# Kernel tuning notes

Measured on AMD Instinct MI355X. Metric: run time of the kernel, lower is better.

The kernel has to match this reference:

```python
import jax, jax.numpy as jnp
import numpy as np

# NF4 codebook (bitsandbytes nf4 data type, 16 levels)
NF4_TABLE = np.array([
    -1.0, -0.6961928009986877, -0.5250730514526367, -0.39491748809814453,
    -0.28444138169288635, -0.18477343022823334, -0.09105003625154495, 0.0,
    0.07958029955625534, 0.16093020141124725, 0.24611230194568634,
    0.33791524171829224, 0.44070982933044434, 0.5626170039176941,
    0.7229568362236023, 1.0], dtype=np.float32)

BLOCKSIZE = 64
SCALING = 32.0 / 16.0  # lora_alpha / r


def setup_inputs() -> dict:
    key = jax.random.key(0)
    k1, k2, k3, k4, k5 = jax.random.split(key, 5)
    tokens, in_f, out_f, r = 256, 4096, 11008, 16
    x = jax.random.normal(k1, (tokens, in_f), dtype=jnp.float32)
    q_codes = jax.random.randint(k2, (out_f, in_f), 0, 16, dtype=jnp.int32)
    absmax = jax.random.uniform(k3, (out_f, in_f // BLOCKSIZE), dtype=jnp.float32)
    lora_A = jax.random.normal(k4, (r, in_f), dtype=jnp.float32) * (1.0 / np.sqrt(in_f))
    lora_B = jax.random.normal(k5, (out_f, r), dtype=jnp.float32) * 0.02
    return {"x": x, "q_codes": q_codes, "absmax": absmax,
            "lora_A": lora_A, "lora_B": lora_B}


def reference(x, q_codes, absmax, lora_A, lora_B):
    out_f, in_f = q_codes.shape
    nf4 = jnp.asarray(NF4_TABLE, dtype=x.dtype)
    # Dequantize: codebook lookup, then per-block absmax scale.
    W = nf4[q_codes].reshape(out_f, in_f // BLOCKSIZE, BLOCKSIZE)
    W = (W * absmax[:, :, None]).reshape(out_f, in_f)  # [out_f, in_f]
    # Base 4-bit linear (no bias in bnb Linear4bit default here).
    base = x @ W.T  # [tokens, out_f]
    # LoRA path: dropout p=0 is identity in eval; scaling = alpha/r.
    lora = (x @ lora_A.T) @ lora_B.T  # [tokens, r] -> [tokens, out_f]
    return base + lora * jnp.asarray(SCALING, dtype=x.dtype)
```

## Files before the change

kernel.cpp:

```cpp
#include <hip/hip_runtime.h>
#include <hip/hip_fp16.h>

typedef unsigned int uint;
typedef unsigned short ushort;

typedef __attribute__((ext_vector_type(8))) _Float16 f16x8;
typedef __attribute__((ext_vector_type(4))) float f32x4;

#define TOK 256
#define OUTF 11008
#define INF 4096
#define BM 256
#define BN 64
#define NT2 172

__device__ __constant__ float NF4_TBL[16] = {
    -1.0f, -0.6961928009986877f, -0.5250730514526367f, -0.39491748809814453f,
    -0.28444138169288635f, -0.18477343022823334f, -0.09105003625154495f, 0.0f,
    0.07958029955625534f, 0.16093020141124725f, 0.24611230194568634f,
    0.33791524171829224f, 0.44070982933044434f, 0.5626170039176941f,
    0.7229568362236023f, 1.0f};

__device__ __forceinline__ ushort f2h(float f) {
  return __half_as_ushort(__float2half(f));
}

__device__ __forceinline__ void async_cp16(const void* g, void* l) {
  __builtin_amdgcn_global_load_lds(
      (const __attribute__((address_space(1))) uint*)g,
      (__attribute__((address_space(3))) uint*)l, 16, 0, 0);
}

__global__ void prep_kernel(const int4* __restrict__ qc4, uint* __restrict__ pk,
                            const float4* __restrict__ x4, ushort4* __restrict__ xh4,
                            const float4* __restrict__ lB4, ushort4* __restrict__ lBh4) {
  const int stride = gridDim.x * blockDim.x;
  const int t0 = blockIdx.x * blockDim.x + threadIdx.x;
  for (int d = t0; d < OUTF * INF / 8; d += stride) {
    int4 a = qc4[2 * d];
    int4 b = qc4[2 * d + 1];
    pk[d] = (uint)(a.x & 15) | ((uint)(a.y & 15) << 4) | ((uint)(a.z & 15) << 8) |
            ((uint)(a.w & 15) << 12) | ((uint)(b.x & 15) << 16) | ((uint)(b.y & 15) << 20) |
            ((uint)(b.z & 15) << 24) | ((uint)(b.w & 15) << 28);
  }
  for (int i = t0; i < TOK * INF / 4; i += stride) {
    float4 v = x4[i];
    ushort4 o;
    o.x = f2h(v.x); o.y = f2h(v.y); o.z = f2h(v.z); o.w = f2h(v.w);
    xh4[i] = o;
  }
  for (int i = t0; i < OUTF * 16; i += stride) {
    int n = i >> 4, jq = i & 15;
    ushort4 o = {0, 0, 0, 0};
    if (jq < 4) {
      float4 v = lB4[n * 4 + jq];
      o.x = f2h(v.x); o.y = f2h(v.y); o.z = f2h(v.z); o.w = f2h(v.w);
    }
    lBh4[i] = o;
  }
}

__global__ __launch_bounds__(1024)
void xa_kernel(const float* __restrict__ x, const float* __restrict__ lA,
               ushort* __restrict__ xa2) {
  const int m = blockIdx.x;
  const int t = threadIdx.x;
  const float4* x4 = (const float4*)(x + (size_t)m * INF);
  const float4* lA4 = (const float4*)lA;
  float4 xv = x4[t];
  float acc[16];
#pragma unroll
  for (int j = 0; j < 16; ++j) {
    float4 a = lA4[j * (INF / 4) + t];
    acc[j] = xv.x * a.x + xv.y * a.y + xv.z * a.z + xv.w * a.w;
  }
#pragma unroll
  for (int j = 0; j < 16; ++j)
#pragma unroll
    for (int s = 32; s > 0; s >>= 1) acc[j] += __shfl_xor(acc[j], s, 64);
  __shared__ float red[16][16];
  const int w = t >> 6, l = t & 63;
  if (l == 0) {
#pragma unroll
    for (int j = 0; j < 16; ++j) red[w][j] = acc[j];
  }
  __syncthreads();
  if (t < 64) {
    ushort v = 0;
    if (t < 16) {
      float s = 0.f;
#pragma unroll
      for (int w2 = 0; w2 < 16; ++w2) s += red[w2][t];
      v = f2h(2.0f * s);
    }
    xa2[m * 64 + t] = v;
  }
}

__global__ __launch_bounds__(256, 3)
void gemm_kernel(const uint* __restrict__ pk, const float* __restrict__ am,
                 const ushort* __restrict__ xh, const ushort* __restrict__ lBh,
                 const ushort* __restrict__ xa2, float* __restrict__ dest, int nst) {
  __shared__ ushort Abuf[BM * 64];
  __shared__ ushort Bbuf[64 * 64];
  __shared__ uint Qbuf[512];
  __shared__ float Qax[1024];
  __shared__ __half2 tbl[256];

  const int tid = threadIdx.x;
  const int w = tid >> 6;
  const int l = tid & 63;
  const int chunk = l >> 4;
  const int rlo = l & 15;
  const int split = blockIdx.x / NT2;
  const int ntile = blockIdx.x - split * NT2;
  const int n0 = ntile * BN;
  const int kb0 = split * nst;

  tbl[tid & 255] = __halves2half2(__float2half(NF4_TBL[tid & 15]),
                                  __float2half(NF4_TBL[(tid >> 4) & 15]));

  const int arow = w * 8 + (l >> 3);
  const int acol = ((l & 7) ^ (l >> 3)) << 3;
  int aoff[2][4];
#pragma unroll
  for (int ks2 = 0; ks2 < 2; ++ks2) {
    const int cc = ks2 * 4 + chunk;
#pragma unroll
    for (int mt = 0; mt < 4; ++mt)
      aoff[ks2][mt] = (w * 64 + mt * 16 + rlo) * 64 + ((cc ^ (l & 7)) << 3);
  }

  const int dr = tid & 63;
  const int p7 = dr & 7;
  const int bw0 = dr * 64 + ((w ^ p7) << 3);
  const int bw1 = dr * 64 + (((w + 4) ^ p7) << 3);

  int boff[2][4];
#pragma unroll
  for (int ks2 = 0; ks2 < 2; ++ks2)
#pragma unroll
    for (int nt = 0; nt < 4; ++nt)
      boff[ks2][nt] = (nt * 16 + rlo) * 64 + (((ks2 * 4 + chunk) ^ (rlo & 7)) << 3);

  f32x4 acc[4][4];
#pragma unroll
  for (int mt = 0; mt < 4; ++mt)
#pragma unroll
    for (int nt = 0; nt < 4; ++nt) acc[mt][nt] = (f32x4){0.f, 0.f, 0.f, 0.f};

  if (w == 0) {
#pragma unroll
    for (int j = 0; j < 4; ++j)
      async_cp16(am + (size_t)(n0 + l) * 64 + kb0 + j * 4, (char*)Qax + j * 1024);
#pragma unroll
    for (int j = 0; j < 2; ++j)
      async_cp16((const char*)pk + (size_t)(n0 + l) * 2048 + kb0 * 32 + j * 16,
                 (char*)Qbuf + j * 1024);
  }
#pragma unroll
  for (int i = 0; i < 8; ++i) {
    const ushort* g = xh + (size_t)(i * 32 + arow) * INF + kb0 * 64 + acol;
    async_cp16(g, &Abuf[(i * 256 + w * 64) * 8]);
  }

  for (int s = 0; s < nst; ++s) {
    __syncthreads();

    uint q0 = Qbuf[dr * 4 + w];
    uint q1 = Qbuf[256 + dr * 4 + w];
    const int sl = s & 15;
    __half2 ax2 = __float2half2_rn(Qax[(sl >> 2) * 256 + dr * 4 + (sl & 3)]);
    {
      union { __half2 h[4]; f16x8 v; } u;
      u.h[0] = __hmul2(tbl[q0 & 255], ax2);
      u.h[1] = __hmul2(tbl[(q0 >> 8) & 255], ax2);
      u.h[2] = __hmul2(tbl[(q0 >> 16) & 255], ax2);
      u.h[3] = __hmul2(tbl[q0 >> 24], ax2);
      *(f16x8*)&Bbuf[bw0] = u.v;
    }
    {
      union { __half2 h[4]; f16x8 v; } u;
      u.h[0] = __hmul2(tbl[q1 & 255], ax2);
      u.h[1] = __hmul2(tbl[(q1 >> 8) & 255], ax2);
      u.h[2] = __hmul2(tbl[(q1 >> 16) & 255], ax2);
      u.h[3] = __hmul2(tbl[q1 >> 24], ax2);
      *(f16x8*)&Bbuf[bw1] = u.v;
    }
    f16x8 areg[2][4];
#pragma unroll
    for (int ks2 = 0; ks2 < 2; ++ks2)
#pragma unroll
      for (int mt = 0; mt < 4; ++mt) areg[ks2][mt] = *(const f16x8*)&Abuf[aoff[ks2][mt]];

    __syncthreads();

    if (s + 1 < nst) {
      const int kb = kb0 + s + 1;
#pragma unroll
      for (int i = 0; i < 8; ++i) {
        const ushort* g = xh + (size_t)(i * 32 + arow) * INF + kb * 64 + acol;
        async_cp16(g, &Abuf[(i * 256 + w * 64) * 8]);
      }
      if (w == 0) {
#pragma unroll
        for (int j = 0; j < 2; ++j)
          async_cp16((const char*)pk + (size_t)(n0 + l) * 2048 + kb * 32 + j * 16,
                     (char*)Qbuf + j * 1024);
        if (((s + 1) & 15) == 0) {
#pragma unroll
          for (int j = 0; j < 4; ++j)
            async_cp16(am + (size_t)(n0 + l) * 64 + kb + j * 4, (char*)Qax + j * 1024);
        }
      }
    }

#pragma unroll
    for (int ks2 = 0; ks2 < 2; ++ks2) {
      f16x8 b[4];
#pragma unroll
      for (int nt = 0; nt < 4; ++nt) b[nt] = *(const f16x8*)&Bbuf[boff[ks2][nt]];
#pragma unroll
      for (int mt = 0; mt < 4; ++mt)
#pragma unroll
        for (int nt = 0; nt < 4; ++nt)
          acc[mt][nt] = __builtin_amdgcn_mfma_f32_16x16x32_f16(areg[ks2][mt], b[nt], acc[mt][nt], 0, 0, 0);
    }
  }

  if (split == 0) {
    f16x8 a_l[4], b_l[4];
#pragma unroll
    for (int mt = 0; mt < 4; ++mt)
      a_l[mt] = *(const f16x8*)(xa2 + (size_t)(w * 64 + mt * 16 + rlo) * 64 + chunk * 8);
#pragma unroll
    for (int nt = 0; nt < 4; ++nt)
      b_l[nt] = *(const f16x8*)(lBh + (size_t)(n0 + nt * 16 + rlo) * 64 + chunk * 8);
#pragma unroll
    for (int mt = 0; mt < 4; ++mt)
#pragma unroll
      for (int nt = 0; nt < 4; ++nt)
        acc[mt][nt] = __builtin_amdgcn_mfma_f32_16x16x32_f16(a_l[mt], b_l[nt], acc[mt][nt], 0, 0, 0);
  }

  float* dst = dest + (size_t)split * TOK * OUTF;
#pragma unroll
  for (int mt = 0; mt < 4; ++mt) {
#pragma unroll
    for (int nt = 0; nt < 4; ++nt) {
      int c = n0 + nt * 16 + rlo;
#pragma unroll
      for (int r = 0; r < 4; ++r) {
        int row = w * 64 + mt * 16 + chunk * 4 + r;
        dst[(size_t)row * OUTF + c] = acc[mt][nt][r];
      }
    }
  }
}

__global__ void reduce_kernel(const float4* __restrict__ part, float4* __restrict__ out,
                              int ks) {
  const int QN = TOK * OUTF / 4;
  int i = blockIdx.x * blockDim.x + threadIdx.x;
  if (i < QN) {
    float4 s = part[i];
    for (int s2 = 1; s2 < ks; ++s2) {
      float4 p = part[(size_t)s2 * QN + i];
      s.x += p.x; s.y += p.y; s.z += p.z; s.w += p.w;
    }
    out[i] = s;
  }
}

extern "C" void kernel_launch(void* const* d_in, const int* in_sizes, int n_in,
                              void* d_out, int out_size, void* d_ws, size_t ws_size,
                              hipStream_t stream) {
  const float* x = (const float*)d_in[0];
  const int* qc = (const int*)d_in[1];
  const float* am = (const float*)d_in[2];
  const float* lA = (const float*)d_in[3];
  const float* lB = (const float*)d_in[4];
  float* out = (float*)d_out;

  const size_t off_lB = (size_t)TOK * INF * 2;
  const size_t off_xa2 = off_lB + (size_t)OUTF * 64 * 2;
  const size_t off_pk = off_xa2 + (size_t)TOK * 64 * 2;
  const size_t off_part = off_pk + (size_t)OUTF * INF / 2;
  const size_t part_bytes = (size_t)TOK * OUTF * 4;

  ushort* xh = (ushort*)d_ws;
  ushort* lBh = (ushort*)((char*)d_ws + off_lB);
  ushort* xa2 = (ushort*)((char*)d_ws + off_xa2);
  uint* pk = (uint*)((char*)d_ws + off_pk);
  float* part = (float*)((char*)d_ws + off_part);

  int ks = 1;
  if (ws_size >= off_part + 4 * part_bytes) ks = 4;
  else if (ws_size >= off_part + 2 * part_bytes) ks = 2;
  float* dest = (ks == 1) ? out : part;

  prep_kernel<<<4096, 256, 0, stream>>>((const int4*)qc, pk, (const float4*)x,
                                        (ushort4*)xh, (const float4*)lB, (ushort4*)lBh);
  xa_kernel<<<TOK, 1024, 0, stream>>>(x, lA, xa2);
  gemm_kernel<<<NT2 * ks, 256, 0, stream>>>(pk, am, xh, lBh, xa2, dest, 64 / ks);
  if (ks > 1)
    reduce_kernel<<<(TOK * OUTF / 4 + 255) / 256, 256, 0, stream>>>((const float4*)part,
                                                                    (float4*)out, ks);
}
```

Baseline: 314.1 us.

## Fuse NF4 code packing into GEMM, dequantizing int32 codes directly via bpermute

Removes the separate pass that packed int32 NF4 codes into nibbles, and has the GEMM load int32 codes into registers each K step, prefetched one step ahead. The codebook lookup moves from an LDS half2 pair table to a ds_bpermute across lanes holding the 16 table values. This eliminates the full read-and-write packing pass over the code matrix. In exchange the GEMM streams 8x more code bytes per tile, and global load latency now sits in registers rather than async LDS copies.

```diff
diff --git a/kernel.cpp b/kernel.cpp
--- a/kernel.cpp
+++ b/kernel.cpp
@@ -31,18 +31,24 @@
       (__attribute__((address_space(3))) uint*)l, 16, 0, 0);
 }
 
-__global__ void prep_kernel(const int4* __restrict__ qc4, uint* __restrict__ pk,
-                            const float4* __restrict__ x4, ushort4* __restrict__ xh4,
+__device__ __forceinline__ float nf4v(int c, int tbits) {
+  return __int_as_float(__builtin_amdgcn_ds_bpermute(c << 2, tbits));
+}
+
+__device__ __forceinline__ uint2 dq4(int4 c, __half2 ax2, int tbits) {
+  __half2 h0 = __floats2half2_rn(nf4v(c.x, tbits), nf4v(c.y, tbits));
+  __half2 h1 = __floats2half2_rn(nf4v(c.z, tbits), nf4v(c.w, tbits));
+  h0 = __hmul2(h0, ax2);
+  h1 = __hmul2(h1, ax2);
+  union { __half2 h[2]; uint2 u; } r;
+  r.h[0] = h0; r.h[1] = h1;
+  return r.u;
+}
+
+__global__ void prep_kernel(const float4* __restrict__ x4, ushort4* __restrict__ xh4,
                             const float4* __restrict__ lB4, ushort4* __restrict__ lBh4) {
   const int stride = gridDim.x * blockDim.x;
   const int t0 = blockIdx.x * blockDim.x + threadIdx.x;
-  for (int d = t0; d < OUTF * INF / 8; d += stride) {
-    int4 a = qc4[2 * d];
-    int4 b = qc4[2 * d + 1];
-    pk[d] = (uint)(a.x & 15) | ((uint)(a.y & 15) << 4) | ((uint)(a.z & 15) << 8) |
-            ((uint)(a.w & 15) << 12) | ((uint)(b.x & 15) << 16) | ((uint)(b.y & 15) << 20) |
-            ((uint)(b.z & 15) << 24) | ((uint)(b.w & 15) << 28);
-  }
   for (int i = t0; i < TOK * INF / 4; i += stride) {
     float4 v = x4[i];
     ushort4 o;
@@ -98,14 +104,12 @@
 }
 
 __global__ __launch_bounds__(256, 3)
-void gemm_kernel(const uint* __restrict__ pk, const float* __restrict__ am,
+void gemm_kernel(const int* __restrict__ qc, const float* __restrict__ am,
                  const ushort* __restrict__ xh, const ushort* __restrict__ lBh,
                  const ushort* __restrict__ xa2, float* __restrict__ dest, int nst) {
   __shared__ ushort Abuf[BM * 64];
   __shared__ ushort Bbuf[64 * 64];
-  __shared__ uint Qbuf[512];
   __shared__ float Qax[1024];
-  __shared__ __half2 tbl[256];
 
   const int tid = threadIdx.x;
   const int w = tid >> 6;
@@ -117,8 +121,7 @@
   const int n0 = ntile * BN;
   const int kb0 = split * nst;
 
-  tbl[tid & 255] = __halves2half2(__float2half(NF4_TBL[tid & 15]),
-                                  __float2half(NF4_TBL[(tid >> 4) & 15]));
+  const int tbits = __float_as_int(NF4_TBL[l & 15]);
 
   const int arow = w * 8 + (l >> 3);
   const int acol = ((l & 7) ^ (l >> 3)) << 3;
@@ -131,10 +134,16 @@
       aoff[ks2][mt] = (w * 64 + mt * 16 + rlo) * 64 + ((cc ^ (l & 7)) << 3);
   }
 
-  const int dr = tid & 63;
-  const int p7 = dr & 7;
-  const int bw0 = dr * 64 + ((w ^ p7) << 3);
-  const int bw1 = dr * 64 + (((w + 4) ^ p7) << 3);
+  const int qrg = tid >> 4;
+  const int qch = tid & 15;
+  const int* qbase[4];
+  int bdst[4];
+#pragma unroll
+  for (int p = 0; p < 4; ++p) {
+    int r = p * 16 + qrg;
+    qbase[p] = qc + (size_t)(n0 + r) * INF + kb0 * 64 + qch * 4;
+    bdst[p] = r * 64 + (((qch >> 1) ^ (r & 7)) << 3) + (qch & 1) * 4;
+  }
 
   int boff[2][4];
 #pragma unroll
@@ -153,39 +162,25 @@
 #pragma unroll
     for (int j = 0; j < 4; ++j)
       async_cp16(am + (size_t)(n0 + l) * 64 + kb0 + j * 4, (char*)Qax + j * 1024);
-#pragma unroll
-    for (int j = 0; j < 2; ++j)
-      async_cp16((const char*)pk + (size_t)(n0 + l) * 2048 + kb0 * 32 + j * 16,
-                 (char*)Qbuf + j * 1024);
   }
 #pragma unroll
   for (int i = 0; i < 8; ++i) {
     const ushort* g = xh + (size_t)(i * 32 + arow) * INF + kb0 * 64 + acol;
     async_cp16(g, &Abuf[(i * 256 + w * 64) * 8]);
   }
+  int4 qreg[4];
+#pragma unroll
+  for (int p = 0; p < 4; ++p) qreg[p] = *(const int4*)(qbase[p]);
 
   for (int s = 0; s < nst; ++s) {
     __syncthreads();
 
-    uint q0 = Qbuf[dr * 4 + w];
-    uint q1 = Qbuf[256 + dr * 4 + w];
     const int sl = s & 15;
-    __half2 ax2 = __float2half2_rn(Qax[(sl >> 2) * 256 + dr * 4 + (sl & 3)]);
-    {
-      union { __half2 h[4]; f16x8 v; } u;
-      u.h[0] = __hmul2(tbl[q0 & 255], ax2);
-      u.h[1] = __hmul2(tbl[(q0 >> 8) & 255], ax2);
-      u.h[2] = __hmul2(tbl[(q0 >> 16) & 255], ax2);
-      u.h[3] = __hmul2(tbl[q0 >> 24], ax2);
-      *(f16x8*)&Bbuf[bw0] = u.v;
-    }
-    {
-      union { __half2 h[4]; f16x8 v; } u;
-      u.h[0] = __hmul2(tbl[q1 & 255], ax2);
-      u.h[1] = __hmul2(tbl[(q1 >> 8) & 255], ax2);
-      u.h[2] = __hmul2(tbl[(q1 >> 16) & 255], ax2);
-      u.h[3] = __hmul2(tbl[q1 >> 24], ax2);
-      *(f16x8*)&Bbuf[bw1] = u.v;
+#pragma unroll
+    for (int p = 0; p < 4; ++p) {
+      int r = p * 16 + qrg;
+      __half2 ax2 = __float2half2_rn(Qax[(sl >> 2) * 256 + r * 4 + (sl & 3)]);
+      *(uint2*)&Bbuf[bdst[p]] = dq4(qreg[p], ax2, tbits);
     }
     f16x8 areg[2][4];
 #pragma unroll
@@ -202,16 +197,12 @@
         const ushort* g = xh + (size_t)(i * 32 + arow) * INF + kb * 64 + acol;
         async_cp16(g, &Abuf[(i * 256 + w * 64) * 8]);
       }
-      if (w == 0) {
-#pragma unroll
-        for (int j = 0; j < 2; ++j)
-          async_cp16((const char*)pk + (size_t)(n0 + l) * 2048 + kb * 32 + j * 16,
-                     (char*)Qbuf + j * 1024);
-        if (((s + 1) & 15) == 0) {
-#pragma unroll
-          for (int j = 0; j < 4; ++j)
-            async_cp16(am + (size_t)(n0 + l) * 64 + kb + j * 4, (char*)Qax + j * 1024);
-        }
+#pragma unroll
+      for (int p = 0; p < 4; ++p) qreg[p] = *(const int4*)(qbase[p] + (s + 1) * 64);
+      if (((s + 1) & 15) == 0 && w == 0) {
+#pragma unroll
+        for (int j = 0; j < 4; ++j)
+          async_cp16(am + (size_t)(n0 + l) * 64 + kb0 + s + 1 + j * 4, (char*)Qax + j * 1024);
       }
     }
 
@@ -284,14 +275,12 @@
 
   const size_t off_lB = (size_t)TOK * INF * 2;
   const size_t off_xa2 = off_lB + (size_t)OUTF * 64 * 2;
-  const size_t off_pk = off_xa2 + (size_t)TOK * 64 * 2;
-  const size_t off_part = off_pk + (size_t)OUTF * INF / 2;
+  const size_t off_part = off_xa2 + (size_t)TOK * 64 * 2;
   const size_t part_bytes = (size_t)TOK * OUTF * 4;
 
   ushort* xh = (ushort*)d_ws;
   ushort* lBh = (ushort*)((char*)d_ws + off_lB);
   ushort* xa2 = (ushort*)((char*)d_ws + off_xa2);
-  uint* pk = (uint*)((char*)d_ws + off_pk);
   float* part = (float*)((char*)d_ws + off_part);
 
   int ks = 1;
@@ -299,10 +288,10 @@
   else if (ws_size >= off_part + 2 * part_bytes) ks = 2;
   float* dest = (ks == 1) ? out : part;
 
-  prep_kernel<<<4096, 256, 0, stream>>>((const int4*)qc, pk, (const float4*)x,
-                                        (ushort4*)xh, (const float4*)lB, (ushort4*)lBh);
+  prep_kernel<<<2048, 256, 0, stream>>>((const float4*)x, (ushort4*)xh,
+                                        (const float4*)lB, (ushort4*)lBh);
   xa_kernel<<<TOK, 1024, 0, stream>>>(x, lA, xa2);
-  gemm_kernel<<<NT2 * ks, 256, 0, stream>>>(pk, am, xh, lBh, xa2, dest, 64 / ks);
+  gemm_kernel<<<NT2 * ks, 256, 0, stream>>>(qc, am, xh, lBh, xa2, dest, 64 / ks);
   if (ks > 1)
     reduce_kernel<<<(TOK * OUTF / 4 + 255) / 256, 256, 0, stream>>>((const float4*)part,
                                                                     (float4*)out, ks);
```

Result: no change. 309.4 us (-1.5%).

## Load A fragments directly from global and double-buffer dequantized B tiles

Applied to the files above, without the earlier changes.

Removes the LDS staging of the activation tile. Each wave now reads its A fragments straight from global memory (L2-resident fp16 x) into registers inside the MFMA loop. The dequantized weight tile, packed codes and absmax buffers become double-buffered, so the next step's B is dequantized before the current MMAs with one barrier per iteration instead of two. This cuts LDS footprint and synchronization, but exposes global load latency on the A operand inside the compute loop.

```diff
diff --git a/kernel.cpp b/kernel.cpp
--- a/kernel.cpp
+++ b/kernel.cpp
@@ -10,7 +10,6 @@
 #define TOK 256
 #define OUTF 11008
 #define INF 4096
-#define BM 256
 #define BN 64
 #define NT2 172
 
@@ -101,10 +100,9 @@
 void gemm_kernel(const uint* __restrict__ pk, const float* __restrict__ am,
                  const ushort* __restrict__ xh, const ushort* __restrict__ lBh,
                  const ushort* __restrict__ xa2, float* __restrict__ dest, int nst) {
-  __shared__ ushort Abuf[BM * 64];
-  __shared__ ushort Bbuf[64 * 64];
-  __shared__ uint Qbuf[512];
-  __shared__ float Qax[1024];
+  __shared__ ushort Bbuf[2][64 * 64];
+  __shared__ uint Qbuf[2][512];
+  __shared__ float Qax[2][1024];
   __shared__ __half2 tbl[256];
 
   const int tid = threadIdx.x;
@@ -120,16 +118,10 @@
   tbl[tid & 255] = __halves2half2(__float2half(NF4_TBL[tid & 15]),
                                   __float2half(NF4_TBL[(tid >> 4) & 15]));
 
-  const int arow = w * 8 + (l >> 3);
-  const int acol = ((l & 7) ^ (l >> 3)) << 3;
-  int aoff[2][4];
-#pragma unroll
-  for (int ks2 = 0; ks2 < 2; ++ks2) {
-    const int cc = ks2 * 4 + chunk;
-#pragma unroll
-    for (int mt = 0; mt < 4; ++mt)
-      aoff[ks2][mt] = (w * 64 + mt * 16 + rlo) * 64 + ((cc ^ (l & 7)) << 3);
-  }
+  const ushort* aptr[4];
+#pragma unroll
+  for (int mt = 0; mt < 4; ++mt)
+    aptr[mt] = xh + (size_t)(w * 64 + mt * 16 + rlo) * INF + chunk * 8 + kb0 * 64;
 
   const int dr = tid & 63;
   const int p7 = dr & 7;
@@ -152,79 +144,82 @@
   if (w == 0) {
 #pragma unroll
     for (int j = 0; j < 4; ++j)
-      async_cp16(am + (size_t)(n0 + l) * 64 + kb0 + j * 4, (char*)Qax + j * 1024);
+      async_cp16(am + (size_t)(n0 + l) * 64 + kb0 + j * 4, (char*)&Qax[0][0] + j * 1024);
 #pragma unroll
     for (int j = 0; j < 2; ++j)
-      async_cp16((const char*)pk + (size_t)(n0 + l) * 2048 + kb0 * 32 + j * 16,
-                 (char*)Qbuf + j * 1024);
-  }
-#pragma unroll
-  for (int i = 0; i < 8; ++i) {
-    const ushort* g = xh + (size_t)(i * 32 + arow) * INF + kb0 * 64 + acol;
-    async_cp16(g, &Abuf[(i * 256 + w * 64) * 8]);
+      async_cp16((const char*)pk + (size_t)(n0 + l) * 2048 + (size_t)kb0 * 32 + j * 16,
+                 (char*)&Qbuf[0][0] + j * 1024);
+  }
+  __syncthreads();
+  {
+    uint q0 = Qbuf[0][dr * 4 + w];
+    uint q1 = Qbuf[0][256 + dr * 4 + w];
+    __half2 ax2 = __float2half2_rn(Qax[0][dr * 4]);
+    union { __half2 h[4]; f16x8 v; } u;
+    u.h[0] = __hmul2(tbl[q0 & 255], ax2);
+    u.h[1] = __hmul2(tbl[(q0 >> 8) & 255], ax2);
+    u.h[2] = __hmul2(tbl[(q0 >> 16) & 255], ax2);
+    u.h[3] = __hmul2(tbl[q0 >> 24], ax2);
+    *(f16x8*)&Bbuf[0][bw0] = u.v;
+    u.h[0] = __hmul2(tbl[q1 & 255], ax2);
+    u.h[1] = __hmul2(tbl[(q1 >> 8) & 255], ax2);
+    u.h[2] = __hmul2(tbl[(q1 >> 16) & 255], ax2);
+    u.h[3] = __hmul2(tbl[q1 >> 24], ax2);
+    *(f16x8*)&Bbuf[0][bw1] = u.v;
+  }
+  if (w == 0 && nst > 1) {
+#pragma unroll
+    for (int j = 0; j < 2; ++j)
+      async_cp16((const char*)pk + (size_t)(n0 + l) * 2048 + (size_t)(kb0 + 1) * 32 + j * 16,
+                 (char*)&Qbuf[1][0] + j * 1024);
   }
 
   for (int s = 0; s < nst; ++s) {
+    const int p = s & 1;
     __syncthreads();
 
-    uint q0 = Qbuf[dr * 4 + w];
-    uint q1 = Qbuf[256 + dr * 4 + w];
-    const int sl = s & 15;
-    __half2 ax2 = __float2half2_rn(Qax[(sl >> 2) * 256 + dr * 4 + (sl & 3)]);
-    {
+    if (s + 1 < nst) {
+      const int t1 = s + 1;
+      uint q0 = Qbuf[p ^ 1][dr * 4 + w];
+      uint q1 = Qbuf[p ^ 1][256 + dr * 4 + w];
+      __half2 ax2 = __float2half2_rn(Qax[(t1 >> 4) & 1][((t1 & 15) >> 2) * 256 + dr * 4 + (t1 & 3)]);
       union { __half2 h[4]; f16x8 v; } u;
       u.h[0] = __hmul2(tbl[q0 & 255], ax2);
       u.h[1] = __hmul2(tbl[(q0 >> 8) & 255], ax2);
       u.h[2] = __hmul2(tbl[(q0 >> 16) & 255], ax2);
       u.h[3] = __hmul2(tbl[q0 >> 24], ax2);
-      *(f16x8*)&Bbuf[bw0] = u.v;
-    }
-    {
-      union { __half2 h[4]; f16x8 v; } u;
+      *(f16x8*)&Bbuf[p ^ 1][bw0] = u.v;
       u.h[0] = __hmul2(tbl[q1 & 255], ax2);
       u.h[1] = __hmul2(tbl[(q1 >> 8) & 255], ax2);
       u.h[2] = __hmul2(tbl[(q1 >> 16) & 255], ax2);
       u.h[3] = __hmul2(tbl[q1 >> 24], ax2);
-      *(f16x8*)&Bbuf[bw1] = u.v;
-    }
-    f16x8 areg[2][4];
-#pragma unroll
-    for (int ks2 = 0; ks2 < 2; ++ks2)
-#pragma unroll
-      for (int mt = 0; mt < 4; ++mt) areg[ks2][mt] = *(const f16x8*)&Abuf[aoff[ks2][mt]];
-
-    __syncthreads();
-
-    if (s + 1 < nst) {
-      const int kb = kb0 + s + 1;
-#pragma unroll
-      for (int i = 0; i < 8; ++i) {
-        const ushort* g = xh + (size_t)(i * 32 + arow) * INF + kb * 64 + acol;
-        async_cp16(g, &Abuf[(i * 256 + w * 64) * 8]);
+      *(f16x8*)&Bbuf[p ^ 1][bw1] = u.v;
+    }
+    if (w == 0 && s + 2 < nst) {
+#pragma unroll
+      for (int j = 0; j < 2; ++j)
+        async_cp16((const char*)pk + (size_t)(n0 + l) * 2048 + (size_t)(kb0 + s + 2) * 32 + j * 16,
+                   (char*)&Qbuf[p][0] + j * 1024);
+      if (((s + 2) & 15) == 0) {
+#pragma unroll
+        for (int j = 0; j < 4; ++j)
+          async_cp16(am + (size_t)(n0 + l) * 64 + kb0 + s + 2 + j * 4,
+                     (char*)&Qax[((s + 2) >> 4) & 1][0] + j * 1024);
       }
-      if (w == 0) {
-#pragma unroll
-        for (int j = 0; j < 2; ++j)
-          async_cp16((const char*)pk + (size_t)(n0 + l) * 2048 + kb * 32 + j * 16,
-                     (char*)Qbuf + j * 1024);
-        if (((s + 1) & 15) == 0) {
-#pragma unroll
-          for (int j = 0; j < 4; ++j)
-            async_cp16(am + (size_t)(n0 + l) * 64 + kb + j * 4, (char*)Qax + j * 1024);
-        }
-      }
     }
 
 #pragma unroll
     for (int ks2 = 0; ks2 < 2; ++ks2) {
-      f16x8 b[4];
-#pragma unroll
-      for (int nt = 0; nt < 4; ++nt) b[nt] = *(const f16x8*)&Bbuf[boff[ks2][nt]];
+      f16x8 a[4], b[4];
+#pragma unroll
+      for (int mt = 0; mt < 4; ++mt) a[mt] = *(const f16x8*)(aptr[mt] + s * 64 + ks2 * 32);
+#pragma unroll
+      for (int nt = 0; nt < 4; ++nt) b[nt] = *(const f16x8*)&Bbuf[p][boff[ks2][nt]];
 #pragma unroll
       for (int mt = 0; mt < 4; ++mt)
 #pragma unroll
         for (int nt = 0; nt < 4; ++nt)
-          acc[mt][nt] = __builtin_amdgcn_mfma_f32_16x16x32_f16(areg[ks2][mt], b[nt], acc[mt][nt], 0, 0, 0);
+          acc[mt][nt] = __builtin_amdgcn_mfma_f32_16x16x32_f16(a[mt], b[nt], acc[mt][nt], 0, 0, 0);
     }
   }
 
```

Result: slower. 335.3 us (+6.8%).

## Merge xa kernel into prep kernel and double-buffer packed NF4 codes

Applied to the files above, without the earlier changes.

Folds the x·A^T LoRA kernel into the prep kernel as extra 256-thread blocks, removing one launch and letting the two run concurrently. In the GEMM, the packed-code buffer Qbuf is double-buffered so the next step's codes are prefetched at the start of each iteration instead of after the second barrier. This is meant to hide global-load latency for the codes at the cost of 2KB more LDS per block, which may affect occupancy.

```diff
diff --git a/kernel.cpp b/kernel.cpp
--- a/kernel.cpp
+++ b/kernel.cpp
@@ -13,6 +13,7 @@
 #define BM 256
 #define BN 64
 #define NT2 172
+#define PREP_BLKS 4096
 
 __device__ __constant__ float NF4_TBL[16] = {
     -1.0f, -0.6961928009986877f, -0.5250730514526367f, -0.39491748809814453f,
@@ -31,69 +32,75 @@
       (__attribute__((address_space(3))) uint*)l, 16, 0, 0);
 }
 
-__global__ void prep_kernel(const int4* __restrict__ qc4, uint* __restrict__ pk,
-                            const float4* __restrict__ x4, ushort4* __restrict__ xh4,
-                            const float4* __restrict__ lB4, ushort4* __restrict__ lBh4) {
-  const int stride = gridDim.x * blockDim.x;
-  const int t0 = blockIdx.x * blockDim.x + threadIdx.x;
-  for (int d = t0; d < OUTF * INF / 8; d += stride) {
-    int4 a = qc4[2 * d];
-    int4 b = qc4[2 * d + 1];
-    pk[d] = (uint)(a.x & 15) | ((uint)(a.y & 15) << 4) | ((uint)(a.z & 15) << 8) |
-            ((uint)(a.w & 15) << 12) | ((uint)(b.x & 15) << 16) | ((uint)(b.y & 15) << 20) |
-            ((uint)(b.z & 15) << 24) | ((uint)(b.w & 15) << 28);
-  }
-  for (int i = t0; i < TOK * INF / 4; i += stride) {
-    float4 v = x4[i];
-    ushort4 o;
-    o.x = f2h(v.x); o.y = f2h(v.y); o.z = f2h(v.z); o.w = f2h(v.w);
-    xh4[i] = o;
-  }
-  for (int i = t0; i < OUTF * 16; i += stride) {
-    int n = i >> 4, jq = i & 15;
-    ushort4 o = {0, 0, 0, 0};
-    if (jq < 4) {
-      float4 v = lB4[n * 4 + jq];
+__global__ __launch_bounds__(256)
+void prep_kernel(const int4* __restrict__ qc4, uint* __restrict__ pk,
+                 const float4* __restrict__ x4, ushort4* __restrict__ xh4,
+                 const float4* __restrict__ lB4, ushort4* __restrict__ lBh4,
+                 const float* __restrict__ x, const float* __restrict__ lA,
+                 ushort* __restrict__ xa2) {
+  if (blockIdx.x < PREP_BLKS) {
+    const int stride = PREP_BLKS * blockDim.x;
+    const int t0 = blockIdx.x * blockDim.x + threadIdx.x;
+    for (int d = t0; d < OUTF * INF / 8; d += stride) {
+      int4 a = qc4[2 * d];
+      int4 b = qc4[2 * d + 1];
+      pk[d] = (uint)(a.x & 15) | ((uint)(a.y & 15) << 4) | ((uint)(a.z & 15) << 8) |
+              ((uint)(a.w & 15) << 12) | ((uint)(b.x & 15) << 16) |
+              ((uint)(b.y & 15) << 20) | ((uint)(b.z & 15) << 24) |
+              ((uint)(b.w & 15) << 28);
+    }
+    for (int i = t0; i < TOK * INF / 4; i += stride) {
+      float4 v = x4[i];
+      ushort4 o;
       o.x = f2h(v.x); o.y = f2h(v.y); o.z = f2h(v.z); o.w = f2h(v.w);
-    }
-    lBh4[i] = o;
-  }
-}
-
-__global__ __launch_bounds__(1024)
-void xa_kernel(const float* __restrict__ x, const float* __restrict__ lA,
-               ushort* __restrict__ xa2) {
-  const int m = blockIdx.x;
-  const int t = threadIdx.x;
-  const float4* x4 = (const float4*)(x + (size_t)m * INF);
-  const float4* lA4 = (const float4*)lA;
-  float4 xv = x4[t];
-  float acc[16];
-#pragma unroll
-  for (int j = 0; j < 16; ++j) {
-    float4 a = lA4[j * (INF / 4) + t];
-    acc[j] = xv.x * a.x + xv.y * a.y + xv.z * a.z + xv.w * a.w;
-  }
-#pragma unroll
-  for (int j = 0; j < 16; ++j)
-#pragma unroll
-    for (int s = 32; s > 0; s >>= 1) acc[j] += __shfl_xor(acc[j], s, 64);
-  __shared__ float red[16][16];
-  const int w = t >> 6, l = t & 63;
-  if (l == 0) {
-#pragma unroll
-    for (int j = 0; j < 16; ++j) red[w][j] = acc[j];
-  }
-  __syncthreads();
-  if (t < 64) {
-    ushort v = 0;
-    if (t < 16) {
-      float s = 0.f;
-#pragma unroll
-      for (int w2 = 0; w2 < 16; ++w2) s += red[w2][t];
-      v = f2h(2.0f * s);
-    }
-    xa2[m * 64 + t] = v;
+      xh4[i] = o;
+    }
+    for (int i = t0; i < OUTF * 16; i += stride) {
+      int n = i >> 4, jq = i & 15;
+      ushort4 o = {0, 0, 0, 0};
+      if (jq < 4) {
+        float4 v = lB4[n * 4 + jq];
+        o.x = f2h(v.x); o.y = f2h(v.y); o.z = f2h(v.z); o.w = f2h(v.w);
+      }
+      lBh4[i] = o;
+    }
+  } else {
+    const int m = blockIdx.x - PREP_BLKS;
+    const int t = threadIdx.x;
+    const float4* xm4 = (const float4*)(x + (size_t)m * INF);
+    const float4* lA4 = (const float4*)lA;
+    float4 xv[4];
+#pragma unroll
+    for (int c = 0; c < 4; ++c) xv[c] = xm4[c * 256 + t];
+    float acc[16];
+#pragma unroll
+    for (int j = 0; j < 16; ++j) {
+      acc[j] = 0.f;
+#pragma unroll
+      for (int c = 0; c < 4; ++c) {
+        float4 a = lA4[j * (INF / 4) + c * 256 + t];
+        acc[j] += xv[c].x * a.x + xv[c].y * a.y + xv[c].z * a.z + xv[c].w * a.w;
+      }
+    }
+#pragma unroll
+    for (int j = 0; j < 16; ++j)
+#pragma unroll
+      for (int s = 32; s > 0; s >>= 1) acc[j] += __shfl_xor(acc[j], s, 64);
+    __shared__ float red[4][16];
+    const int w = t >> 6, l = t & 63;
+    if (l == 0) {
+#pragma unroll
+      for (int j = 0; j < 16; ++j) red[w][j] = acc[j];
+    }
+    __syncthreads();
+    if (t < 64) {
+      ushort v = 0;
+      if (t < 16) {
+        float s = red[0][t] + red[1][t] + red[2][t] + red[3][t];
+        v = f2h(2.0f * s);
+      }
+      xa2[m * 64 + t] = v;
+    }
   }
 }
 
@@ -103,7 +110,7 @@
                  const ushort* __restrict__ xa2, float* __restrict__ dest, int nst) {
   __shared__ ushort Abuf[BM * 64];
   __shared__ ushort Bbuf[64 * 64];
-  __shared__ uint Qbuf[512];
+  __shared__ uint Qbuf[2][512];
   __shared__ float Qax[1024];
   __shared__ __half2 tbl[256];
 
@@ -155,8 +162,8 @@
       async_cp16(am + (size_t)(n0 + l) * 64 + kb0 + j * 4, (char*)Qax + j * 1024);
 #pragma unroll
     for (int j = 0; j < 2; ++j)
-      async_cp16((const char*)pk + (size_t)(n0 + l) * 2048 + kb0 * 32 + j * 16,
-                 (char*)Qbuf + j * 1024);
+      async_cp16((const char*)pk + (size_t)(n0 + l) * 2048 + (size_t)kb0 * 32 + j * 16,
+                 (char*)&Qbuf[0][0] + j * 1024);
   }
 #pragma unroll
   for (int i = 0; i < 8; ++i) {
@@ -165,22 +172,27 @@
   }
 
   for (int s = 0; s < nst; ++s) {
+    const int p = s & 1;
     __syncthreads();
 
-    uint q0 = Qbuf[dr * 4 + w];
-    uint q1 = Qbuf[256 + dr * 4 + w];
-    const int sl = s & 15;
-    __half2 ax2 = __float2half2_rn(Qax[(sl >> 2) * 256 + dr * 4 + (sl & 3)]);
+    if (w == 0 && s + 1 < nst) {
+#pragma unroll
+      for (int j = 0; j < 2; ++j)
+        async_cp16((const char*)pk + (size_t)(n0 + l) * 2048 + (size_t)(kb0 + s + 1) * 32 + j * 16,
+                   (char*)&Qbuf[p ^ 1][0] + j * 1024);
+    }
+
     {
+      const int sl = s & 15;
+      uint q0 = Qbuf[p][dr * 4 + w];
+      uint q1 = Qbuf[p][256 + dr * 4 + w];
+      __half2 ax2 = __float2half2_rn(Qax[(sl >> 2) * 256 + dr * 4 + (sl & 3)]);
       union { __half2 h[4]; f16x8 v; } u;
       u.h[0] = __hmul2(tbl[q0 & 255], ax2);
       u.h[1] = __hmul2(tbl[(q0 >> 8) & 255], ax2);
       u.h[2] = __hmul2(tbl[(q0 >> 16) & 255], ax2);
       u.h[3] = __hmul2(tbl[q0 >> 24], ax2);
       *(f16x8*)&Bbuf[bw0] = u.v;
-    }
-    {
-      union { __half2 h[4]; f16x8 v; } u;
       u.h[0] = __hmul2(tbl[q1 & 255], ax2);
       u.h[1] = __hmul2(tbl[(q1 >> 8) & 255], ax2);
       u.h[2] = __hmul2(tbl[(q1 >> 16) & 255], ax2);
@@ -202,16 +214,10 @@
         const ushort* g = xh + (size_t)(i * 32 + arow) * INF + kb * 64 + acol;
         async_cp16(g, &Abuf[(i * 256 + w * 64) * 8]);
       }
-      if (w == 0) {
-#pragma unroll
-        for (int j = 0; j < 2; ++j)
-          async_cp16((const char*)pk + (size_t)(n0 + l) * 2048 + kb * 32 + j * 16,
-                     (char*)Qbuf + j * 1024);
-        if (((s + 1) & 15) == 0) {
-#pragma unroll
-          for (int j = 0; j < 4; ++j)
-            async_cp16(am + (size_t)(n0 + l) * 64 + kb + j * 4, (char*)Qax + j * 1024);
-        }
+      if (w == 0 && ((s + 1) & 15) == 0) {
+#pragma unroll
+        for (int j = 0; j < 4; ++j)
+          async_cp16(am + (size_t)(n0 + l) * 64 + kb + j * 4, (char*)Qax + j * 1024);
       }
     }
 
@@ -299,9 +305,9 @@
   else if (ws_size >= off_part + 2 * part_bytes) ks = 2;
   float* dest = (ks == 1) ? out : part;
 
-  prep_kernel<<<4096, 256, 0, stream>>>((const int4*)qc, pk, (const float4*)x,
-                                        (ushort4*)xh, (const float4*)lB, (ushort4*)lBh);
-  xa_kernel<<<TOK, 1024, 0, stream>>>(x, lA, xa2);
+  prep_kernel<<<PREP_BLKS + TOK, 256, 0, stream>>>(
+      (const int4*)qc, pk, (const float4*)x, (ushort4*)xh,
+      (const float4*)lB, (ushort4*)lBh, x, lA, xa2);
   gemm_kernel<<<NT2 * ks, 256, 0, stream>>>(pk, am, xh, lBh, xa2, dest, 64 / ks);
   if (ks > 1)
     reduce_kernel<<<(TOK * OUTF / 4 + 255) / 256, 256, 0, stream>>>((const float4*)part,
```

Measured after the change: 314.2 us. About the same (+0.0%).
